# Performance work log

Measured on AMD Instinct MI355X. Metric: run time of the kernel, lower is better.

Reference implementation:

```python
import jax, jax.numpy as jnp
import numpy as np
from jax import lax

IN_DIM, HID_DIM, OUT_DIM = 1024, 2048, 1024
N_EXP_A, TOPK_A, N_EXP_G = 12, 4, 6
BATCH = 2048
# Shannon entropy (nats) of {1/2, 1/3, 1/6}
H_TARGET = float(-(0.5 * np.log(0.5) + (1.0 / 3.0) * np.log(1.0 / 3.0) + (1.0 / 6.0) * np.log(1.0 / 6.0)))


def setup_inputs() -> dict:
    key = jax.random.key(0)
    ks = jax.random.split(key, 24)
    s_in = 1.0 / np.sqrt(IN_DIM)
    s_hid = 1.0 / np.sqrt(HID_DIM)
    s_out = 1.0 / np.sqrt(OUT_DIM)
    d = {}
    d['x'] = jax.random.normal(ks[0], (BATCH, IN_DIM), dtype=jnp.float32)
    # EngineA: gate + 12 experts (stacked)
    d['gate_a_w'] = jax.random.normal(ks[1], (IN_DIM, N_EXP_A), jnp.float32) * s_in
    d['gate_a_b'] = jnp.zeros((N_EXP_A,), jnp.float32)
    d['wa1'] = jax.random.normal(ks[2], (N_EXP_A, IN_DIM, HID_DIM), jnp.float32) * s_in
    d['ba1'] = jnp.zeros((N_EXP_A, HID_DIM), jnp.float32)
    d['wa2'] = jax.random.normal(ks[3], (N_EXP_A, HID_DIM, OUT_DIM), jnp.float32) * s_hid
    d['ba2'] = jnp.zeros((N_EXP_A, OUT_DIM), jnp.float32)
    # EngineG: gate + 6 experts (stacked)
    d['gate_g_w'] = jax.random.normal(ks[4], (IN_DIM, N_EXP_G), jnp.float32) * s_in
    d['gate_g_b'] = jnp.zeros((N_EXP_G,), jnp.float32)
    d['wg1'] = jax.random.normal(ks[5], (N_EXP_G, IN_DIM, HID_DIM), jnp.float32) * s_in
    d['bg1'] = jnp.zeros((N_EXP_G, HID_DIM), jnp.float32)
    d['wg2'] = jax.random.normal(ks[6], (N_EXP_G, HID_DIM, OUT_DIM), jnp.float32) * s_hid
    d['bg2'] = jnp.zeros((N_EXP_G, OUT_DIM), jnp.float32)
    # self_model: Linear(3,hid) Tanh Linear(hid,out) Tanh
    d['sm_w1'] = jax.random.normal(ks[7], (3, HID_DIM), jnp.float32) * (1.0 / np.sqrt(3.0))
    d['sm_b1'] = jnp.zeros((HID_DIM,), jnp.float32)
    d['sm_w2'] = jax.random.normal(ks[8], (HID_DIM, OUT_DIM), jnp.float32) * s_hid
    d['sm_b2'] = jnp.zeros((OUT_DIM,), jnp.float32)
    # self_influence Linear(out,out)
    d['si_w'] = jax.random.normal(ks[9], (OUT_DIM, OUT_DIM), jnp.float32) * s_out
    d['si_b'] = jnp.zeros((OUT_DIM,), jnp.float32)
    # field_transform Linear(out,out) + Tanh
    d['ft_w'] = jax.random.normal(ks[10], (OUT_DIM, OUT_DIM), jnp.float32) * s_out
    d['ft_b'] = jnp.zeros((OUT_DIM,), jnp.float32)
    d['tension_scale'] = jnp.asarray(1.0 / 3.0, jnp.float32)
    d['n_steps'] = 3
    return d


def _experts(x, w1, b1, w2, b2):
    # x:[B,I], w1:[E,I,H] -> [B,E,O]  (Linear-ReLU-Linear per expert)
    h = jax.nn.relu(jnp.einsum('bi,eih->beh', x, w1) + b1[None])
    return jnp.einsum('beh,eho->beo', h, w2) + b2[None]


def reference(x, gate_a_w, gate_a_b, wa1, ba1, wa2, ba2,
              gate_g_w, gate_g_b, wg1, bg1, wg2, bg2,
              sm_w1, sm_b1, sm_w2, sm_b2, si_w, si_b, ft_w, ft_b,
              tension_scale, n_steps):
    B = x.shape[0]
    # ---- EngineA: top-k (k=4 of 12) MoE ----
    logits_a = x @ gate_a_w + gate_a_b
    topv, topi = lax.top_k(logits_a, TOPK_A)
    topw = jax.nn.softmax(topv, axis=-1)
    weights_a = jnp.zeros_like(logits_a).at[jnp.arange(B)[:, None], topi].set(topw)
    out_a = _experts(x, wa1, ba1, wa2, ba2)            # [B,12,O]
    out_plus = jnp.einsum('be,beo->bo', weights_a, out_a)
    # ---- EngineG: dense-softmax MoE + entropy loss ----
    weights_g = jax.nn.softmax(x @ gate_g_w + gate_g_b, axis=-1)
    out_g = _experts(x, wg1, bg1, wg2, bg2)            # [B,6,O]
    out_minus = jnp.einsum('be,beo->bo', weights_g, out_g)
    h_ent = -(weights_g * jnp.log(weights_g + 1e-8)).sum(-1).mean()
    entropy_loss = (h_ent - H_TARGET) ** 2
    # ---- self-referential loop ----
    repulsion = out_plus - out_minus
    prev_tension = (repulsion ** 2).sum(-1, keepdims=True)      # [B,1]
    tensions = [lax.stop_gradient(prev_tension.mean())]          # .item() detaches
    modified_repulsion = repulsion
    for step in range(n_steps):
        tension_scalar = prev_tension.mean(-1, keepdims=True)    # [B,1]
        if step == 0:
            tension_delta = jnp.zeros_like(tension_scalar)
        else:
            tension_delta = tension_scalar - tensions[-1]
        step_tensor = jnp.full_like(tension_scalar, step / n_steps)
        self_input = jnp.concatenate([tension_scalar, tension_delta, step_tensor], -1)  # [B,3]
        self_state = jnp.tanh(jnp.tanh(self_input @ sm_w1 + sm_b1) @ sm_w2 + sm_b2)
        influence = self_state @ si_w + si_b
        modified_repulsion = repulsion + influence
        prev_tension = (modified_repulsion ** 2).sum(-1, keepdims=True)
        tensions.append(lax.stop_gradient(prev_tension.mean()))
    equilibrium = (out_plus + out_minus) * 0.5
    field_direction = jnp.tanh(modified_repulsion @ ft_w + ft_b)
    output = equilibrium + tension_scale * jnp.sqrt(prev_tension + 1e-8) * field_direction
    t = jnp.stack(tensions)
    convergence_loss = jnp.abs(t[1:] - t[:-1]).mean()            # built from .item()s -> constant
    aux_loss = entropy_loss + 0.001 * convergence_loss
    return output, aux_loss
```

## Files before the change

kernel.cpp:

```cpp
#include <hip/hip_runtime.h>

typedef _Float16 f16;
typedef f16  f16x8 __attribute__((ext_vector_type(8)));
typedef f16  f16x4 __attribute__((ext_vector_type(4)));
typedef float f32x4 __attribute__((ext_vector_type(4)));

#define LOAD_LDS16(gp, lp) __builtin_amdgcn_global_load_lds( \
    (const __attribute__((address_space(1))) void*)(gp),     \
    (__attribute__((address_space(3))) void*)(lp), 16, 0, 0)

#define BARX() __builtin_amdgcn_s_barrier()
#define SB0() __builtin_amdgcn_sched_barrier(0)
#define WLG0() asm volatile("s_waitcnt lgkmcnt(0)" ::: "memory")
#define WVM8() asm volatile("s_waitcnt vmcnt(8)" ::: "memory")
#define WVM0() asm volatile("s_waitcnt vmcnt(0)" ::: "memory")

#define ST_A(TT, BB, KH) { \
  const long ko_ = (long)((TT) < NKC ? (TT) : (NKC - 1)) * 64 + (KH) * 32; \
  LOAD_LDS16(pa0 + ko_, &Al[BB][KH][tid * 8]); \
  LOAD_LDS16(pa1 + ko_, &Al[BB][KH][(512 + tid) * 8]); }
#define ST_B(TT, BB, KH) { \
  const long ko_ = (long)((TT) < NKC ? (TT) : (NKC - 1)) * 64 + (KH) * 32; \
  LOAD_LDS16(pb0 + ko_, &Bl[BB][KH][tid * 8]); \
  LOAD_LDS16(pb1 + ko_, &Bl[BB][KH][(512 + tid) * 8]); }

#define RD_AV(BB, KH) _Pragma("unroll") \
  for (int i_ = 0; i_ < 8; i_++) \
    av[i_] = *(const f16x8*)&Al[BB][KH][(arow + i_ * 16) * 32 + qa];
#define RD_BV(BB, KH, CB) _Pragma("unroll") \
  for (int j_ = 0; j_ < 2; j_++) \
    bv[j_] = *(const f16x8*)&Bl[BB][KH][(brow + (CB) * 32 + j_ * 16) * 32 + qa];
#define MF16(CB) \
  __builtin_amdgcn_s_setprio(1); \
  _Pragma("unroll") \
  for (int i_ = 0; i_ < 8; i_++) { \
    acc[i_][2 * (CB)]     = __builtin_amdgcn_mfma_f32_16x16x32_f16(av[i_], bv[0], acc[i_][2 * (CB)], 0, 0, 0); \
    acc[i_][2 * (CB) + 1] = __builtin_amdgcn_mfma_f32_16x16x32_f16(av[i_], bv[1], acc[i_][2 * (CB) + 1], 0, 0, 0); \
  } \
  __builtin_amdgcn_s_setprio(0);

#define GTILE(KT, BUF) { \
  RD_AV(BUF, 0) RD_BV(BUF, 0, 0) \
  ST_A((KT) + 1, (BUF) ^ 1, 1) \
  BARX(); WLG0(); SB0(); \
  MF16(0) \
  SB0(); BARX(); \
  RD_BV(BUF, 0, 1) \
  ST_B((KT) + 1, (BUF) ^ 1, 1) \
  WVM8(); \
  BARX(); WLG0(); SB0(); \
  MF16(1) \
  SB0(); BARX(); \
  RD_AV(BUF, 1) RD_BV(BUF, 1, 0) \
  ST_A((KT) + 2, (BUF), 0) \
  BARX(); WLG0(); SB0(); \
  MF16(0) \
  SB0(); BARX(); \
  RD_BV(BUF, 1, 1) \
  ST_B((KT) + 2, (BUF), 0) \
  WVM8(); \
  BARX(); WLG0(); SB0(); \
  MF16(1) \
  SB0(); BARX(); \
}


__global__ __launch_bounds__(256) void transpose_cast2(const float* __restrict__ s0,
                                                       const float* __restrict__ s1,
                                                       int zsplit, f16* __restrict__ dst,
                                                       int R, int C, long sbatch,
                                                       long dbatch, int dld) {
  __shared__ float tile[32][33];
  const int zc = blockIdx.x * 32;
  const int zr = blockIdx.y * 32;
  const int z  = blockIdx.z;
  const float* s = (z < zsplit) ? (s0 + (long)z * sbatch)
                                : (s1 + (long)(z - zsplit) * sbatch);
  f16* d = dst + (long)z * dbatch;
  const int tx = threadIdx.x & 31, ty = threadIdx.x >> 5;
#pragma unroll
  for (int rr = 0; rr < 32; rr += 8)
    tile[ty + rr][tx] = s[(long)(zr + ty + rr) * C + (zc + tx)];
  __syncthreads();
#pragma unroll
  for (int rr = 0; rr < 32; rr += 8)
    d[(long)(zc + ty + rr) * dld + (zr + tx)] = (f16)tile[tx][ty + rr];
}

struct TDesc { const float* s; f16* d; int R; int C; int dld; };
struct TDesc3 { TDesc m[3]; };

__global__ __launch_bounds__(256) void transpose3(TDesc3 p) {
  const TDesc t = p.m[blockIdx.z];
  const int zc = blockIdx.x * 32;
  const int zr = blockIdx.y * 32;
  if (zr >= t.R || zc >= t.C) return;
  __shared__ float tile[32][33];
  const int tx = threadIdx.x & 31, ty = threadIdx.x >> 5;
#pragma unroll
  for (int rr = 0; rr < 32; rr += 8)
    tile[ty + rr][tx] = t.s[(long)(zr + ty + rr) * t.C + (zc + tx)];
  __syncthreads();
#pragma unroll
  for (int rr = 0; rr < 32; rr += 8)
    t.d[(long)(zc + ty + rr) * t.dld + (zr + tx)] = (f16)tile[tx][ty + rr];
}

__global__ __launch_bounds__(256) void gating_kernel(
    const float* __restrict__ x, const float* __restrict__ gaw,
    const float* __restrict__ gab, const float* __restrict__ ggw,
    const float* __restrict__ ggb, f16* __restrict__ xb,
    float* __restrict__ wG, float* __restrict__ ent,
    int* __restrict__ rows, float* __restrict__ gval, int* __restrict__ cnt,
    int* __restrict__ eA, int* __restrict__ posA, float* __restrict__ wA4) {
  const int b = blockIdx.x, t = threadIdx.x;
  const float* xr = x + (long)b * 1024;
  float pa[12], pg[6];
#pragma unroll
  for (int e = 0; e < 12; e++) pa[e] = 0.f;
#pragma unroll
  for (int e = 0; e < 6; e++) pg[e] = 0.f;
  const int i0 = t * 4;
  const float4 xv = *(const float4*)(xr + i0);
  f16x4 hx; hx.x = (f16)xv.x; hx.y = (f16)xv.y; hx.z = (f16)xv.z; hx.w = (f16)xv.w;
  *(f16x4*)(xb + (long)b * 1024 + i0) = hx;
  const float xs[4] = {xv.x, xv.y, xv.z, xv.w};
#pragma unroll
  for (int u = 0; u < 4; u++) {
    const float xi = xs[u];
    const float* ga = gaw + (long)(i0 + u) * 12;
    const float* gg = ggw + (long)(i0 + u) * 6;
#pragma unroll
    for (int e = 0; e < 12; e++) pa[e] += xi * ga[e];
#pragma unroll
    for (int e = 0; e < 6; e++) pg[e] += xi * gg[e];
  }
#pragma unroll
  for (int e = 0; e < 12; e++)
    for (int m = 1; m < 64; m <<= 1) pa[e] += __shfl_xor(pa[e], m);
#pragma unroll
  for (int e = 0; e < 6; e++)
    for (int m = 1; m < 64; m <<= 1) pg[e] += __shfl_xor(pg[e], m);
  __shared__ float rw[4][18];
  const int lane = t & 63, wv = t >> 6;
  if (lane == 0) {
#pragma unroll
    for (int e = 0; e < 12; e++) rw[wv][e] = pa[e];
#pragma unroll
    for (int e = 0; e < 6; e++) rw[wv][12 + e] = pg[e];
  }
  __syncthreads();
  if (t == 0) {
    float la[12], lg[6];
#pragma unroll
    for (int e = 0; e < 12; e++)
      la[e] = rw[0][e] + rw[1][e] + rw[2][e] + rw[3][e] + gab[e];
#pragma unroll
    for (int e = 0; e < 6; e++)
      lg[e] = rw[0][12 + e] + rw[1][12 + e] + rw[2][12 + e] + rw[3][12 + e] + ggb[e];
    unsigned used = 0; float tv[4]; int tix[4];
    for (int k = 0; k < 4; k++) {
      float best = -3.4e38f; int bi = 0;
      for (int e = 0; e < 12; e++)
        if (!((used >> e) & 1u) && la[e] > best) { best = la[e]; bi = e; }
      tv[k] = best; tix[k] = bi; used |= 1u << bi;
    }
    const float mx = tv[0];
    float s = 0.f, w4[4];
    for (int k = 0; k < 4; k++) { w4[k] = expf(tv[k] - mx); s += w4[k]; }
    for (int k = 0; k < 4; k++) {
      const float w = w4[k] / s;
      const int e = tix[k];
      const int pos = atomicAdd(&cnt[e], 1);
      rows[e * 2048 + pos] = b;
      gval[e * 2048 + pos] = w;
      eA[b * 4 + k] = e;
      posA[b * 4 + k] = pos;
      wA4[b * 4 + k] = w;
    }
    float mg = lg[0];
    for (int e = 1; e < 6; e++) mg = fmaxf(mg, lg[e]);
    float sg = 0.f, wg6[6];
    for (int e = 0; e < 6; e++) { wg6[e] = expf(lg[e] - mg); sg += wg6[e]; }
    float H = 0.f;
    for (int e = 0; e < 6; e++) {
      const float w = wg6[e] / sg;
      wG[b * 6 + e] = w;
      H -= w * logf(w + 1e-8f);
    }
    ent[b] = H;
  }
}

__global__ void base_kernel(const int* __restrict__ cnt, int* __restrict__ baseA) {
  if (threadIdx.x == 0 && blockIdx.x == 0) {
    int r = 0;
    for (int e = 0; e < 12; e++) { baseA[e] = r; r += cnt[e]; }
  }
}

__global__ __launch_bounds__(256) void combine_kernel(
    const f16* __restrict__ res, const int* __restrict__ eA,
    const int* __restrict__ posA, const float* __restrict__ wA4,
    const float* __restrict__ wG, const int* __restrict__ baseA,
    const float* __restrict__ ba2, const float* __restrict__ bg2,
    float* __restrict__ outP, float* __restrict__ outM,
    float* __restrict__ pt0, float* __restrict__ ts0) {
  const long b = blockIdx.x;
  const int t = threadIdx.x;
  const int c = t * 4;
  float4 P = {0.f, 0.f, 0.f, 0.f}, M = {0.f, 0.f, 0.f, 0.f};
#pragma unroll
  for (int k = 0; k < 4; k++) {
    const int e = eA[b * 4 + k];
    const long slot = baseA[e] + posA[b * 4 + k];
    const f16x4 v = *(const f16x4*)(res + slot * 1024 + c);
    const float w = wA4[b * 4 + k];
    const float4 bb = *(const float4*)(ba2 + (long)e * 1024 + c);
    P.x += (float)v.x + w * bb.x; P.y += (float)v.y + w * bb.y;
    P.z += (float)v.z + w * bb.z; P.w += (float)v.w + w * bb.w;
  }
#pragma unroll
  for (int e = 0; e < 6; e++) {
    const f16x4 v = *(const f16x4*)(res + (8192L + e * 2048 + b) * 1024 + c);
    const float w = wG[b * 6 + e];
    const float4 bb = *(const float4*)(bg2 + (long)e * 1024 + c);
    M.x += (float)v.x + w * bb.x; M.y += (float)v.y + w * bb.y;
    M.z += (float)v.z + w * bb.z; M.w += (float)v.w + w * bb.w;
  }
  *(float4*)(outP + b * 1024 + c) = P;
  *(float4*)(outM + b * 1024 + c) = M;
  const float dx = P.x - M.x, dy = P.y - M.y, dz = P.z - M.z, dw = P.w - M.w;
  float s = dx * dx + dy * dy + dz * dz + dw * dw;
#pragma unroll
  for (int m = 1; m < 64; m <<= 1) s += __shfl_xor(s, m);
  __shared__ float rw[4];
  if ((t & 63) == 0) rw[t >> 6] = s;
  __syncthreads();
  if (t == 0) {
    const float tot = rw[0] + rw[1] + rw[2] + rw[3];
    pt0[b] = tot;
    atomicAdd(ts0, tot);
  }
}

__global__ __launch_bounds__(256) void hsm_kernel(
    const float* __restrict__ pt, const float* __restrict__ tsum,
    const float* __restrict__ w1, const float* __restrict__ b1,
    f16* __restrict__ o, int step) {
  const int j = blockIdx.x * 256 + threadIdx.x;
  const int b0 = blockIdx.y * 64;
  const float u0 = w1[j], u1 = w1[2048 + j], u2 = w1[4096 + j], bb = b1[j];
  const float tm = tsum[0] * (1.f / 2048.f);
  const float st = (float)step * (1.f / 3.f);
#pragma unroll 4
  for (int r = 0; r < 64; r++) {
    const int b = b0 + r;
    const float t = pt[b];
    const float delta = (step == 0) ? 0.f : (t - tm);
    o[(long)b * 2048 + j] = (f16)tanhf(t * u0 + delta * u1 + st * u2 + bb);
  }
}

__global__ __launch_bounds__(512, 2) void gemm1_kernel(
    const f16* __restrict__ x, const f16* __restrict__ w1t,
    const float* __restrict__ ba1, const float* __restrict__ bg1,
    f16* __restrict__ h, const int* __restrict__ rows,
    const float* __restrict__ gval, const int* __restrict__ cnt,
    const int* __restrict__ baseA, const float* __restrict__ wG) {
  constexpr int NKC = 16;
  __shared__ f16 Al[2][2][8192];
  __shared__ f16 Bl[2][2][8192];
  __shared__ int   Lrow[256];
  __shared__ float Lg[256];
  int id = blockIdx.x;
  int e18, mi, ni, live; long row0; const float* bp;
  if (id < 768) {
    const int k = id & 7, t = id >> 3;
    mi = t & 7; const int pid = k * 12 + (t >> 3);
    const int e = pid >> 3; ni = pid & 7;
    live = cnt[e] - mi * 256;
    if (live <= 0) return;
    if (live > 256) live = 256;
    row0 = baseA[e] + mi * 256; e18 = e; bp = ba1 + (long)e * 2048;
  } else {
    id -= 768;
    const int k = id & 7, t = id >> 3;
    mi = t & 7; const int pid = k * 6 + (t >> 3);
    const int e = pid >> 3; ni = pid & 7;
    row0 = 8192L + e * 2048 + mi * 256; live = 256;
    e18 = 12 + e; bp = bg1 + (long)e * 2048;
  }
  const int tid = threadIdx.x;
  const bool routed = (e18 < 12);
  if (tid < 256) {
    const int gi = mi * 256 + tid;
    if (routed) {
      const bool ok = tid < live;
      Lrow[tid] = ok ? rows[e18 * 2048 + gi] : 0;
      Lg[tid]   = ok ? gval[e18 * 2048 + gi] : 0.f;
    } else {
      Lrow[tid] = gi;
      Lg[tid] = wG[gi * 6 + (e18 - 12)];
    }
  }
  __syncthreads();
  const int srow = tid >> 2;
  const int sch = ((tid & 3) ^ ((tid >> 3) & 3)) * 8;
  const f16* pa0 = x + (long)Lrow[srow] * 1024 + sch;
  const f16* pa1 = x + (long)Lrow[128 + srow] * 1024 + sch;
  const f16* pb0 = w1t + (long)e18 * 2048 * 1024 + ((long)ni * 256 + srow) * 1024 + sch;
  const f16* pb1 = pb0 + 128 * 1024;
  const int wave = tid >> 6, lane = tid & 63;
  const int wm = wave & 1, wn = wave >> 1;
  const int l16 = lane & 15, q = lane >> 4;
  const int qa = (q ^ ((l16 >> 1) & 3)) * 8;
  const int arow = wm * 128 + l16;
  const int brow = wn * 64 + l16;
  f32x4 acc[8][4] = {};
  f16x8 av[8], bv[2];
  ST_A(0, 0, 0) ST_B(0, 0, 0) ST_A(0, 0, 1) ST_B(0, 0, 1) ST_A(1, 1, 0) ST_B(1, 1, 0)
  WVM8(); BARX(); SB0();
#pragma unroll 1
  for (int kt = 0; kt < NKC; kt += 2) { GTILE(kt, 0) GTILE(kt + 1, 1) }
  WVM0();
#pragma unroll
  for (int i = 0; i < 8; i++) {
#pragma unroll
    for (int r = 0; r < 4; r++) {
      const int lr = wm * 128 + i * 16 + q * 4 + r;
      if (lr < live) {
        const float wv = Lg[lr];
        f16* C = h + (row0 + lr) * 2048 + ni * 256;
#pragma unroll
        for (int jj = 0; jj < 4; jj++) {
          const int cc = wn * 64 + jj * 16 + l16;
          const float v = fmaxf(acc[i][jj][r] + bp[ni * 256 + cc], 0.f) * wv;
          C[cc] = (f16)v;
        }
      }
    }
  }
}

__global__ __launch_bounds__(512, 2) void gemm2_kernel(
    const f16* __restrict__ h, const f16* __restrict__ w2t,
    f16* __restrict__ res, const int* __restrict__ cnt,
    const int* __restrict__ baseA) {
  constexpr int NKC = 32;
  __shared__ f16 Al[2][2][8192];
  __shared__ f16 Bl[2][2][8192];
  int id = blockIdx.x;
  int e18, mi, ni, live; long row0;
  if (id < 384) {
    const int k = id & 7, t = id >> 3;
    mi = t & 7; const int pid = k * 6 + (t >> 3);
    const int e = pid >> 2; ni = pid & 3;
    live = cnt[e] - mi * 256;
    if (live <= 0) return;
    if (live > 256) live = 256;
    row0 = baseA[e] + mi * 256; e18 = e;
  } else {
    id -= 384;
    const int k = id & 7, t = id >> 3;
    mi = t & 7; const int pid = k * 3 + (t >> 3);
    const int e = pid >> 2; ni = pid & 3;
    row0 = 8192L + e * 2048 + mi * 256; live = 256; e18 = 12 + e;
  }
  const int tid = threadIdx.x;
  const int srow = tid >> 2;
  const int sch = ((tid & 3) ^ ((tid >> 3) & 3)) * 8;
  const f16* pa0 = h + (row0 + srow) * 2048 + sch;
  const f16* pa1 = pa0 + 128 * 2048;
  const f16* pb0 = w2t + (long)e18 * 1024 * 2048 + ((long)ni * 256 + srow) * 2048 + sch;
  const f16* pb1 = pb0 + 128 * 2048;
  const int wave = tid >> 6, lane = tid & 63;
  const int wm = wave & 1, wn = wave >> 1;
  const int l16 = lane & 15, q = lane >> 4;
  const int qa = (q ^ ((l16 >> 1) & 3)) * 8;
  const int arow = wm * 128 + l16;
  const int brow = wn * 64 + l16;
  f32x4 acc[8][4] = {};
  f16x8 av[8], bv[2];
  ST_A(0, 0, 0) ST_B(0, 0, 0) ST_A(0, 0, 1) ST_B(0, 0, 1) ST_A(1, 1, 0) ST_B(1, 1, 0)
  WVM8(); BARX(); SB0();
#pragma unroll 1
  for (int kt = 0; kt < NKC; kt += 2) { GTILE(kt, 0) GTILE(kt + 1, 1) }
  WVM0();
#pragma unroll
  for (int i = 0; i < 8; i++) {
#pragma unroll
    for (int r = 0; r < 4; r++) {
      const int lr = wm * 128 + i * 16 + q * 4 + r;
      if (lr < live) {
        f16* C = res + (row0 + lr) * 1024 + ni * 256 + wn * 64 + l16;
#pragma unroll
        for (int jj = 0; jj < 4; jj++) C[jj * 16] = (f16)acc[i][jj][r];
      }
    }
  }
}


struct GA {
  const f16* A; long lda;
  const f16* B; long ldb;
  int nk;
  float* Cf; f16* Ch;
  const float* bias;
  const float* op; const float* om;
  const float* pt; const float* ts;
  float* pt_out; float* tsum_out;
  const float* ent; const float* tsb; float* aux_out;
};

template <int EPI>
__global__ __launch_bounds__(256) void gemm_s(GA a) {
  __shared__ f16 Al[2][64 * 64];
  __shared__ f16 Bl[2][64 * 64];
  const int tid = threadIdx.x;
  const int wave = tid >> 6, lane = tid & 63;
  const int wm = wave & 1, wn = wave >> 1;
  const int l16 = lane & 15, q = lane >> 4;
  const long m0 = (long)blockIdx.y * 64;
  const long n0 = (long)blockIdx.x * 64;
  const int srow = tid >> 3;
  const int sch  = ((tid & 7) ^ (srow & 7)) * 8;
  const f16* a0 = a.A + (m0 + srow) * a.lda + sch;
  const f16* a1 = a.A + (m0 + srow + 32) * a.lda + sch;
  const f16* b0 = a.B + (n0 + srow) * a.ldb + sch;
  const f16* b1 = a.B + (n0 + srow + 32) * a.ldb + sch;
  const int rx = (l16 & 7) * 8;
  f32x4 acc[2][2] = {};
  LOAD_LDS16(a0, &Al[0][tid * 8]);
  LOAD_LDS16(a1, &Al[0][(256 + tid) * 8]);
  LOAD_LDS16(b0, &Bl[0][tid * 8]);
  LOAD_LDS16(b1, &Bl[0][(256 + tid) * 8]);
  for (int kk = 0; kk < a.nk; ++kk) {
    __syncthreads();
    const int cur = kk & 1;
    if (kk + 1 < a.nk) {
      const long k0 = (long)(kk + 1) * 64;
      const int nb = cur ^ 1;
      LOAD_LDS16(a0 + k0, &Al[nb][tid * 8]);
      LOAD_LDS16(a1 + k0, &Al[nb][(256 + tid) * 8]);
      LOAD_LDS16(b0 + k0, &Bl[nb][tid * 8]);
      LOAD_LDS16(b1 + k0, &Bl[nb][(256 + tid) * 8]);
    }
    f16x8 avv[2][2], bvv[2][2];
#pragma unroll
    for (int hf = 0; hf < 2; hf++) {
      const int cA = (((hf * 4 + q) * 8) ^ rx);
#pragma unroll
      for (int i = 0; i < 2; i++)
        avv[hf][i] = *(const f16x8*)&Al[cur][(wm * 32 + i * 16 + l16) * 64 + cA];
#pragma unroll
      for (int j = 0; j < 2; j++)
        bvv[hf][j] = *(const f16x8*)&Bl[cur][(wn * 32 + j * 16 + l16) * 64 + cA];
    }
#pragma unroll
    for (int hf = 0; hf < 2; hf++)
#pragma unroll
      for (int i = 0; i < 2; i++)
#pragma unroll
        for (int j = 0; j < 2; j++)
          acc[i][j] = __builtin_amdgcn_mfma_f32_16x16x32_f16(avv[hf][i], bvv[hf][j], acc[i][j], 0, 0, 0);
  }
  if constexpr (EPI == 2) {
#pragma unroll
    for (int i = 0; i < 2; i++)
#pragma unroll
      for (int r = 0; r < 4; r++) {
        const long gr = m0 + wm * 32 + i * 16 + q * 4 + r;
#pragma unroll
        for (int j = 0; j < 2; j++) {
          const int gc = (int)n0 + wn * 32 + j * 16 + l16;
          a.Ch[gr * 1024 + gc] = (f16)tanhf(acc[i][j][r] + a.bias[gc]);
        }
      }
  } else if constexpr (EPI == 3) {
    float wave_ss = 0.f;
#pragma unroll
    for (int i = 0; i < 2; i++)
#pragma unroll
      for (int r = 0; r < 4; r++) {
        const long gr = m0 + wm * 32 + i * 16 + q * 4 + r;
        float ss = 0.f;
#pragma unroll
        for (int j = 0; j < 2; j++) {
          const int gc = (int)n0 + wn * 32 + j * 16 + l16;
          const long ix = gr * 1024 + gc;
          const float v = (a.op[ix] - a.om[ix]) + acc[i][j][r] + a.bias[gc];
          a.Ch[ix] = (f16)v;
          ss += v * v;
        }
        ss += __shfl_xor(ss, 1); ss += __shfl_xor(ss, 2);
        ss += __shfl_xor(ss, 4); ss += __shfl_xor(ss, 8);
        if (l16 == 0) {
          atomicAdd(a.pt_out + gr, ss);
          wave_ss += ss;
        }
      }
    wave_ss += __shfl_xor(wave_ss, 16);
    wave_ss += __shfl_xor(wave_ss, 32);
    if (lane == 0) atomicAdd(a.tsum_out, wave_ss);
  } else {
    const float tsc = a.ts[0];
#pragma unroll
    for (int i = 0; i < 2; i++)
#pragma unroll
      for (int r = 0; r < 4; r++) {
        const long gr = m0 + wm * 32 + i * 16 + q * 4 + r;
        const float sq = sqrtf(a.pt[gr] + 1e-8f) * tsc;
#pragma unroll
        for (int j = 0; j < 2; j++) {
          const int gc = (int)n0 + wn * 32 + j * 16 + l16;
          const long ix = gr * 1024 + gc;
          const float v = tanhf(acc[i][j][r] + a.bias[gc]);
          a.Cf[ix] = 0.5f * (a.op[ix] + a.om[ix]) + sq * v;
        }
      }
    if (blockIdx.x == 0 && blockIdx.y == 0) {
      float s = 0.f;
      for (int i = tid; i < 2048; i += 256) s += a.ent[i];
#pragma unroll
      for (int m = 1; m < 64; m <<= 1) s += __shfl_xor(s, m);
      __shared__ float rwa[4];
      if ((tid & 63) == 0) rwa[tid >> 6] = s;
      __syncthreads();
      if (tid == 0) {
        const float hh = (rwa[0] + rwa[1] + rwa[2] + rwa[3]) * (1.f / 2048.f);
        const float dd = hh - 1.0114042647f;
        const float el = dd * dd;
        const float t0 = a.tsb[0] * (1.f / 2048.f), t1 = a.tsb[1] * (1.f / 2048.f);
        const float t2 = a.tsb[2] * (1.f / 2048.f), t3 = a.tsb[3] * (1.f / 2048.f);
        const float conv = (fabsf(t1 - t0) + fabsf(t2 - t1) + fabsf(t3 - t2)) * (1.f / 3.f);
        a.aux_out[0] = el + 0.001f * conv;
      }
    }
  }
}


extern "C" void kernel_launch(void* const* d_in, const int* in_sizes, int n_in,
                              void* d_out, int out_size, void* d_ws, size_t ws_size,
                              hipStream_t stream) {
  (void)in_sizes; (void)n_in; (void)out_size; (void)ws_size;
  const float* x    = (const float*)d_in[0];
  const float* gaw  = (const float*)d_in[1];
  const float* gab  = (const float*)d_in[2];
  const float* wa1  = (const float*)d_in[3];
  const float* ba1  = (const float*)d_in[4];
  const float* wa2  = (const float*)d_in[5];
  const float* ba2  = (const float*)d_in[6];
  const float* ggw  = (const float*)d_in[7];
  const float* ggb  = (const float*)d_in[8];
  const float* wg1  = (const float*)d_in[9];
  const float* bg1  = (const float*)d_in[10];
  const float* wg2  = (const float*)d_in[11];
  const float* bg2  = (const float*)d_in[12];
  const float* smw1 = (const float*)d_in[13];
  const float* smb1 = (const float*)d_in[14];
  const float* smw2 = (const float*)d_in[15];
  const float* smb2 = (const float*)d_in[16];
  const float* siw  = (const float*)d_in[17];
  const float* sib  = (const float*)d_in[18];
  const float* ftw  = (const float*)d_in[19];
  const float* ftb  = (const float*)d_in[20];
  const float* tsc  = (const float*)d_in[21];

  char* p = (char*)d_ws;
  size_t off = 0;
  auto alloc = [&](size_t bytes) -> char* {
    char* r = p + off;
    off = (off + bytes + 255) & ~(size_t)255;
    return r;
  };
  f16* xb     = (f16*)alloc(2048UL * 1024 * 2);
  f16* w1t    = (f16*)alloc(18UL * 2048 * 1024 * 2);
  f16* smw2t  = (f16*)alloc(1024UL * 2048 * 2);
  f16* sit    = (f16*)alloc(1024UL * 1024 * 2);
  f16* ftt    = (f16*)alloc(1024UL * 1024 * 2);
  f16* h      = (f16*)alloc(20480UL * 2048 * 2);
  f16* res    = (f16*)alloc(20480UL * 1024 * 2);
  float* outP = (float*)alloc(2048UL * 1024 * 4);
  float* outM = (float*)alloc(2048UL * 1024 * 4);
  f16* hsmb   = (f16*)alloc(2048UL * 2048 * 2);
  f16* sst    = (f16*)alloc(2048UL * 1024 * 2);
  f16* modb   = (f16*)alloc(2048UL * 1024 * 2);
  float* entb = (float*)alloc(2048 * 4);
  float* wGb  = (float*)alloc(2048 * 6 * 4);
  float* ptb  = (float*)alloc(4 * 2048 * 4);
  float* tsb  = (float*)alloc(4 * 4);
  int*   cntb = (int*)alloc(12 * 4);
  int*   baseAb = (int*)alloc(12 * 4);
  int*   rowsb  = (int*)alloc(12 * 2048 * 4);
  float* gvalb  = (float*)alloc(12 * 2048 * 4);
  int*   eAb    = (int*)alloc(2048 * 4 * 4);
  int*   posAb  = (int*)alloc(2048 * 4 * 4);
  float* wA4b   = (float*)alloc(2048 * 4 * 4);

  f16* w2t = w1t;

  hipMemsetAsync(ptb, 0, 33072, stream);

  transpose_cast2<<<dim3(64, 32, 18), 256, 0, stream>>>(wa1, wg1, 12, w1t,
      1024, 2048, 1024L * 2048, 2048L * 1024, 1024);
  {
    TDesc3 td;
    td.m[0] = {smw2, smw2t, 2048, 1024, 2048};
    td.m[1] = {siw,  sit,  1024, 1024, 1024};
    td.m[2] = {ftw,  ftt,  1024, 1024, 1024};
    transpose3<<<dim3(32, 64, 3), 256, 0, stream>>>(td);
  }
  gating_kernel<<<2048, 256, 0, stream>>>(x, gaw, gab, ggw, ggb, xb, wGb, entb,
                                          rowsb, gvalb, cntb, eAb, posAb, wA4b);
  base_kernel<<<1, 64, 0, stream>>>(cntb, baseAb);

  gemm1_kernel<<<1152, 512, 0, stream>>>(xb, w1t, ba1, bg1, h,
                                         rowsb, gvalb, cntb, baseAb, wGb);

  transpose_cast2<<<dim3(32, 64, 18), 256, 0, stream>>>(wa2, wg2, 12, w2t,
      2048, 1024, 2048L * 1024, 1024L * 2048, 2048);

  gemm2_kernel<<<576, 512, 0, stream>>>(h, w2t, res, cntb, baseAb);

  combine_kernel<<<2048, 256, 0, stream>>>(res, eAb, posAb, wA4b, wGb, baseAb,
                                           ba2, bg2, outP, outM, ptb, tsb);

  for (int s = 0; s < 3; s++) {
    hsm_kernel<<<dim3(8, 32), 256, 0, stream>>>(ptb + s * 2048, tsb + s, smw1, smb1, hsmb, s);
    GA g3{};
    g3.A = hsmb; g3.lda = 2048; g3.B = smw2t; g3.ldb = 2048; g3.nk = 32;
    g3.Ch = sst; g3.bias = smb2;
    gemm_s<2><<<dim3(16, 32), 256, 0, stream>>>(g3);
    GA g4{};
    g4.A = sst; g4.lda = 1024; g4.B = sit; g4.ldb = 1024; g4.nk = 16;
    g4.Ch = modb; g4.bias = sib; g4.op = outP; g4.om = outM;
    g4.pt_out = ptb + (s + 1) * 2048; g4.tsum_out = tsb + (s + 1);
    gemm_s<3><<<dim3(16, 32), 256, 0, stream>>>(g4);
  }

  GA g5{};
  g5.A = modb; g5.lda = 1024; g5.B = ftt; g5.ldb = 1024; g5.nk = 16;
  g5.Cf = (float*)d_out; g5.bias = ftb; g5.op = outP; g5.om = outM;
  g5.pt = ptb + 3 * 2048; g5.ts = tsc;
  g5.ent = entb; g5.tsb = tsb; g5.aux_out = (float*)d_out + 2048UL * 1024;
  gemm_s<4><<<dim3(16, 32), 256, 0, stream>>>(g5);
}
```

Measured before the change: 999.5 us.

## Use persistent atomic work-queue blocks for expert GEMMs and reorder MFMA register blocking

Both grouped expert GEMM kernels now launch a fixed grid of 256 persistent blocks. Each block pulls tile indices from a global atomic counter held in the zeroed scratch buffer, so empty routed tiles are skipped cheaply and the load balances across CUs instead of running on an oversized grid with early exits. The inner MFMA schedule is also reorganized: each phase loads four A fragments and four B fragments and does a 4x4 block of MFMAs, in place of eight A fragments against two B fragments. This changes LDS read volume and register pressure. The trade-off is atomic and barrier overhead per tile, plus reliance on the memset covering the counter offset.

Result: no change. 1.005 ms (+0.5%).

```diff
diff --git a/kernel.cpp b/kernel.cpp
--- a/kernel.cpp
+++ b/kernel.cpp
@@ -24,43 +24,43 @@
   LOAD_LDS16(pb0 + ko_, &Bl[BB][KH][tid * 8]); \
   LOAD_LDS16(pb1 + ko_, &Bl[BB][KH][(512 + tid) * 8]); }
 
-#define RD_AV(BB, KH) _Pragma("unroll") \
-  for (int i_ = 0; i_ < 8; i_++) \
-    av[i_] = *(const f16x8*)&Al[BB][KH][(arow + i_ * 16) * 32 + qa];
-#define RD_BV(BB, KH, CB) _Pragma("unroll") \
-  for (int j_ = 0; j_ < 2; j_++) \
-    bv[j_] = *(const f16x8*)&Bl[BB][KH][(brow + (CB) * 32 + j_ * 16) * 32 + qa];
-#define MF16(CB) \
+#define RD_A4(DST, BB, KH, HB) _Pragma("unroll") \
+  for (int i_ = 0; i_ < 4; i_++) \
+    DST[i_] = *(const f16x8*)&Al[BB][KH][(arow + (HB) * 64 + i_ * 16) * 32 + qa];
+#define RD_B4(BB, KH) _Pragma("unroll") \
+  for (int j_ = 0; j_ < 4; j_++) \
+    bvv[j_] = *(const f16x8*)&Bl[BB][KH][(brow + j_ * 16) * 32 + qa];
+#define MFC(AV, OFF) \
   __builtin_amdgcn_s_setprio(1); \
   _Pragma("unroll") \
-  for (int i_ = 0; i_ < 8; i_++) { \
-    acc[i_][2 * (CB)]     = __builtin_amdgcn_mfma_f32_16x16x32_f16(av[i_], bv[0], acc[i_][2 * (CB)], 0, 0, 0); \
-    acc[i_][2 * (CB) + 1] = __builtin_amdgcn_mfma_f32_16x16x32_f16(av[i_], bv[1], acc[i_][2 * (CB) + 1], 0, 0, 0); \
-  } \
+  for (int i_ = 0; i_ < 4; i_++) \
+    _Pragma("unroll") \
+    for (int j_ = 0; j_ < 4; j_++) \
+      acc[(OFF) + i_][j_] = __builtin_amdgcn_mfma_f32_16x16x32_f16(AV[i_], bvv[j_], acc[(OFF) + i_][j_], 0, 0, 0); \
   __builtin_amdgcn_s_setprio(0);
 
 #define GTILE(KT, BUF) { \
-  RD_AV(BUF, 0) RD_BV(BUF, 0, 0) \
+  RD_A4(ava, BUF, 0, 0) RD_B4(BUF, 0) \
   ST_A((KT) + 1, (BUF) ^ 1, 1) \
   BARX(); WLG0(); SB0(); \
-  MF16(0) \
+  MFC(ava, 0) \
   SB0(); BARX(); \
-  RD_BV(BUF, 0, 1) \
+  RD_A4(avb, BUF, 0, 1) \
   ST_B((KT) + 1, (BUF) ^ 1, 1) \
   WVM8(); \
   BARX(); WLG0(); SB0(); \
-  MF16(1) \
+  MFC(avb, 4) \
   SB0(); BARX(); \
-  RD_AV(BUF, 1) RD_BV(BUF, 1, 0) \
+  RD_A4(ava, BUF, 1, 0) RD_B4(BUF, 1) \
   ST_A((KT) + 2, (BUF), 0) \
   BARX(); WLG0(); SB0(); \
-  MF16(0) \
+  MFC(ava, 0) \
   SB0(); BARX(); \
-  RD_BV(BUF, 1, 1) \
+  RD_A4(avb, BUF, 1, 1) \
   ST_B((KT) + 2, (BUF), 0) \
   WVM8(); \
   BARX(); WLG0(); SB0(); \
-  MF16(1) \
+  MFC(avb, 4) \
   SB0(); BARX(); \
 }
 
@@ -267,76 +267,83 @@
     const float* __restrict__ ba1, const float* __restrict__ bg1,
     f16* __restrict__ h, const int* __restrict__ rows,
     const float* __restrict__ gval, const int* __restrict__ cnt,
-    const int* __restrict__ baseA, const float* __restrict__ wG) {
+    const int* __restrict__ baseA, const float* __restrict__ wG,
+    int* __restrict__ wq) {
   constexpr int NKC = 16;
   __shared__ f16 Al[2][2][8192];
   __shared__ f16 Bl[2][2][8192];
   __shared__ int   Lrow[256];
   __shared__ float Lg[256];
-  int id = blockIdx.x;
-  int e18, mi, ni, live; long row0; const float* bp;
-  if (id < 768) {
-    const int k = id & 7, t = id >> 3;
-    mi = t & 7; const int pid = k * 12 + (t >> 3);
-    const int e = pid >> 3; ni = pid & 7;
-    live = cnt[e] - mi * 256;
-    if (live <= 0) return;
-    if (live > 256) live = 256;
-    row0 = baseA[e] + mi * 256; e18 = e; bp = ba1 + (long)e * 2048;
-  } else {
-    id -= 768;
-    const int k = id & 7, t = id >> 3;
-    mi = t & 7; const int pid = k * 6 + (t >> 3);
-    const int e = pid >> 3; ni = pid & 7;
-    row0 = 8192L + e * 2048 + mi * 256; live = 256;
-    e18 = 12 + e; bp = bg1 + (long)e * 2048;
-  }
+  __shared__ int qv;
   const int tid = threadIdx.x;
-  const bool routed = (e18 < 12);
-  if (tid < 256) {
-    const int gi = mi * 256 + tid;
-    if (routed) {
-      const bool ok = tid < live;
-      Lrow[tid] = ok ? rows[e18 * 2048 + gi] : 0;
-      Lg[tid]   = ok ? gval[e18 * 2048 + gi] : 0.f;
-    } else {
-      Lrow[tid] = gi;
-      Lg[tid] = wG[gi * 6 + (e18 - 12)];
-    }
-  }
-  __syncthreads();
   const int srow = tid >> 2;
   const int sch = ((tid & 3) ^ ((tid >> 3) & 3)) * 8;
-  const f16* pa0 = x + (long)Lrow[srow] * 1024 + sch;
-  const f16* pa1 = x + (long)Lrow[128 + srow] * 1024 + sch;
-  const f16* pb0 = w1t + (long)e18 * 2048 * 1024 + ((long)ni * 256 + srow) * 1024 + sch;
-  const f16* pb1 = pb0 + 128 * 1024;
   const int wave = tid >> 6, lane = tid & 63;
   const int wm = wave & 1, wn = wave >> 1;
-  const int l16 = lane & 15, q = lane >> 4;
-  const int qa = (q ^ ((l16 >> 1) & 3)) * 8;
+  const int l16 = lane & 15, qt = lane >> 4;
+  const int qa = (qt ^ ((l16 >> 1) & 3)) * 8;
   const int arow = wm * 128 + l16;
   const int brow = wn * 64 + l16;
-  f32x4 acc[8][4] = {};
-  f16x8 av[8], bv[2];
-  ST_A(0, 0, 0) ST_B(0, 0, 0) ST_A(0, 0, 1) ST_B(0, 0, 1) ST_A(1, 1, 0) ST_B(1, 1, 0)
-  WVM8(); BARX(); SB0();
+  for (;;) {
+    if (tid == 0) qv = atomicAdd(wq, 1);
+    __syncthreads();
+    int id = qv;
+    if (id >= 1152) return;
+    int e18, mi, ni, live; long row0; const float* bp;
+    if (id < 768) {
+      const int k = id & 7, t = id >> 3;
+      mi = t & 7; const int pid = k * 12 + (t >> 3);
+      const int e = pid >> 3; ni = pid & 7;
+      live = cnt[e] - mi * 256;
+      if (live > 256) live = 256;
+      row0 = baseA[e] + mi * 256; e18 = e; bp = ba1 + (long)e * 2048;
+    } else {
+      const int id2 = id - 768;
+      const int k = id2 & 7, t = id2 >> 3;
+      mi = t & 7; const int pid = k * 6 + (t >> 3);
+      const int e = pid >> 3; ni = pid & 7;
+      row0 = 8192L + e * 2048 + mi * 256; live = 256;
+      e18 = 12 + e; bp = bg1 + (long)e * 2048;
+    }
+    if (live <= 0) continue;
+    const bool routed = (e18 < 12);
+    if (tid < 256) {
+      const int gi = mi * 256 + tid;
+      if (routed) {
+        const bool ok = tid < live;
+        Lrow[tid] = ok ? rows[e18 * 2048 + gi] : 0;
+        Lg[tid]   = ok ? gval[e18 * 2048 + gi] : 0.f;
+      } else {
+        Lrow[tid] = gi;
+        Lg[tid] = wG[gi * 6 + (e18 - 12)];
+      }
+    }
+    __syncthreads();
+    const f16* pa0 = x + (long)Lrow[srow] * 1024 + sch;
+    const f16* pa1 = x + (long)Lrow[128 + srow] * 1024 + sch;
+    const f16* pb0 = w1t + (long)e18 * 2048 * 1024 + ((long)ni * 256 + srow) * 1024 + sch;
+    const f16* pb1 = pb0 + 128 * 1024;
+    f32x4 acc[8][4] = {};
+    f16x8 ava[4], avb[4], bvv[4];
+    ST_A(0, 0, 0) ST_B(0, 0, 0) ST_A(0, 0, 1) ST_B(0, 0, 1) ST_A(1, 1, 0) ST_B(1, 1, 0)
+    WVM8(); BARX(); SB0();
 #pragma unroll 1
-  for (int kt = 0; kt < NKC; kt += 2) { GTILE(kt, 0) GTILE(kt + 1, 1) }
-  WVM0();
-#pragma unroll
-  for (int i = 0; i < 8; i++) {
-#pragma unroll
-    for (int r = 0; r < 4; r++) {
-      const int lr = wm * 128 + i * 16 + q * 4 + r;
-      if (lr < live) {
-        const float wv = Lg[lr];
-        f16* C = h + (row0 + lr) * 2048 + ni * 256;
-#pragma unroll
-        for (int jj = 0; jj < 4; jj++) {
-          const int cc = wn * 64 + jj * 16 + l16;
-          const float v = fmaxf(acc[i][jj][r] + bp[ni * 256 + cc], 0.f) * wv;
-          C[cc] = (f16)v;
+    for (int kt = 0; kt < NKC; kt += 2) { GTILE(kt, 0) GTILE(kt + 1, 1) }
+    WVM0();
+#pragma unroll
+    for (int i = 0; i < 8; i++) {
+#pragma unroll
+      for (int r = 0; r < 4; r++) {
+        const int lr = wm * 128 + i * 16 + qt * 4 + r;
+        if (lr < live) {
+          const float wv = Lg[lr];
+          f16* C = h + (row0 + lr) * 2048 + ni * 256;
+#pragma unroll
+          for (int jj = 0; jj < 4; jj++) {
+            const int cc = wn * 64 + jj * 16 + l16;
+            const float v = fmaxf(acc[i][jj][r] + bp[ni * 256 + cc], 0.f) * wv;
+            C[cc] = (f16)v;
+          }
         }
       }
     }
@@ -346,56 +353,62 @@
 __global__ __launch_bounds__(512, 2) void gemm2_kernel(
     const f16* __restrict__ h, const f16* __restrict__ w2t,
     f16* __restrict__ res, const int* __restrict__ cnt,
-    const int* __restrict__ baseA) {
+    const int* __restrict__ baseA, int* __restrict__ wq) {
   constexpr int NKC = 32;
   __shared__ f16 Al[2][2][8192];
   __shared__ f16 Bl[2][2][8192];
-  int id = blockIdx.x;
-  int e18, mi, ni, live; long row0;
-  if (id < 384) {
-    const int k = id & 7, t = id >> 3;
-    mi = t & 7; const int pid = k * 6 + (t >> 3);
-    const int e = pid >> 2; ni = pid & 3;
-    live = cnt[e] - mi * 256;
-    if (live <= 0) return;
-    if (live > 256) live = 256;
-    row0 = baseA[e] + mi * 256; e18 = e;
-  } else {
-    id -= 384;
-    const int k = id & 7, t = id >> 3;
-    mi = t & 7; const int pid = k * 3 + (t >> 3);
-    const int e = pid >> 2; ni = pid & 3;
-    row0 = 8192L + e * 2048 + mi * 256; live = 256; e18 = 12 + e;
-  }
+  __shared__ int qv;
   const int tid = threadIdx.x;
   const int srow = tid >> 2;
   const int sch = ((tid & 3) ^ ((tid >> 3) & 3)) * 8;
-  const f16* pa0 = h + (row0 + srow) * 2048 + sch;
-  const f16* pa1 = pa0 + 128 * 2048;
-  const f16* pb0 = w2t + (long)e18 * 1024 * 2048 + ((long)ni * 256 + srow) * 2048 + sch;
-  const f16* pb1 = pb0 + 128 * 2048;
   const int wave = tid >> 6, lane = tid & 63;
   const int wm = wave & 1, wn = wave >> 1;
-  const int l16 = lane & 15, q = lane >> 4;
-  const int qa = (q ^ ((l16 >> 1) & 3)) * 8;
+  const int l16 = lane & 15, qt = lane >> 4;
+  const int qa = (qt ^ ((l16 >> 1) & 3)) * 8;
   const int arow = wm * 128 + l16;
   const int brow = wn * 64 + l16;
-  f32x4 acc[8][4] = {};
-  f16x8 av[8], bv[2];
-  ST_A(0, 0, 0) ST_B(0, 0, 0) ST_A(0, 0, 1) ST_B(0, 0, 1) ST_A(1, 1, 0) ST_B(1, 1, 0)
-  WVM8(); BARX(); SB0();
+  for (;;) {
+    if (tid == 0) qv = atomicAdd(wq, 1);
+    __syncthreads();
+    int id = qv;
+    if (id >= 576) return;
+    int e18, mi, ni, live; long row0;
+    if (id < 384) {
+      const int k = id & 7, t = id >> 3;
+      mi = t & 7; const int pid = k * 6 + (t >> 3);
+      const int e = pid >> 2; ni = pid & 3;
+      live = cnt[e] - mi * 256;
+      if (live > 256) live = 256;
+      row0 = baseA[e] + mi * 256; e18 = e;
+    } else {
+      const int id2 = id - 384;
+      const int k = id2 & 7, t = id2 >> 3;
+      mi = t & 7; const int pid = k * 3 + (t >> 3);
+      const int e = pid >> 2; ni = pid & 3;
+      row0 = 8192L + e * 2048 + mi * 256; live = 256; e18 = 12 + e;
+    }
+    if (live <= 0) continue;
+    const f16* pa0 = h + (row0 + srow) * 2048 + sch;
+    const f16* pa1 = pa0 + 128 * 2048;
+    const f16* pb0 = w2t + (long)e18 * 1024 * 2048 + ((long)ni * 256 + srow) * 2048 + sch;
+    const f16* pb1 = pb0 + 128 * 2048;
+    f32x4 acc[8][4] = {};
+    f16x8 ava[4], avb[4], bvv[4];
+    ST_A(0, 0, 0) ST_B(0, 0, 0) ST_A(0, 0, 1) ST_B(0, 0, 1) ST_A(1, 1, 0) ST_B(1, 1, 0)
+    WVM8(); BARX(); SB0();
 #pragma unroll 1
-  for (int kt = 0; kt < NKC; kt += 2) { GTILE(kt, 0) GTILE(kt + 1, 1) }
-  WVM0();
-#pragma unroll
-  for (int i = 0; i < 8; i++) {
-#pragma unroll
-    for (int r = 0; r < 4; r++) {
-      const int lr = wm * 128 + i * 16 + q * 4 + r;
-      if (lr < live) {
-        f16* C = res + (row0 + lr) * 1024 + ni * 256 + wn * 64 + l16;
-#pragma unroll
-        for (int jj = 0; jj < 4; jj++) C[jj * 16] = (f16)acc[i][jj][r];
+    for (int kt = 0; kt < NKC; kt += 2) { GTILE(kt, 0) GTILE(kt + 1, 1) }
+    WVM0();
+#pragma unroll
+    for (int i = 0; i < 8; i++) {
+#pragma unroll
+      for (int r = 0; r < 4; r++) {
+        const int lr = wm * 128 + i * 16 + qt * 4 + r;
+        if (lr < live) {
+          f16* C = res + (row0 + lr) * 1024 + ni * 256 + wn * 64 + l16;
+#pragma unroll
+          for (int jj = 0; jj < 4; jj++) C[jj * 16] = (f16)acc[i][jj][r];
+        }
       }
     }
   }
@@ -601,6 +614,7 @@
   float* wA4b   = (float*)alloc(2048 * 4 * 4);
 
   f16* w2t = w1t;
+  int* qq = (int*)((char*)tsb + 64);
 
   hipMemsetAsync(ptb, 0, 33072, stream);
 
@@ -617,13 +631,13 @@
                                           rowsb, gvalb, cntb, eAb, posAb, wA4b);
   base_kernel<<<1, 64, 0, stream>>>(cntb, baseAb);
 
-  gemm1_kernel<<<1152, 512, 0, stream>>>(xb, w1t, ba1, bg1, h,
-                                         rowsb, gvalb, cntb, baseAb, wGb);
+  gemm1_kernel<<<256, 512, 0, stream>>>(xb, w1t, ba1, bg1, h,
+                                        rowsb, gvalb, cntb, baseAb, wGb, qq);
 
   transpose_cast2<<<dim3(32, 64, 18), 256, 0, stream>>>(wa2, wg2, 12, w2t,
       2048, 1024, 2048L * 1024, 1024L * 2048, 2048);
 
-  gemm2_kernel<<<576, 512, 0, stream>>>(h, w2t, res, cntb, baseAb);
+  gemm2_kernel<<<256, 512, 0, stream>>>(h, w2t, res, cntb, baseAb, qq + 1);
 
   combine_kernel<<<2048, 256, 0, stream>>>(res, eAb, posAb, wA4b, wGb, baseAb,
                                            ba2, bg2, outP, outM, ptb, tsb);
```
